# Kernel tuning notes

Hardware: AMD Instinct MI355X
Metric: run time of the kernel (lower is better)

The kernel has to match this reference:

```python
import jax, jax.numpy as jnp
import numpy as np

TEMPERATURE = 3.0
SINKHORN_ITERS = 20
NOISE_SCALE = 1.0
EPS = 1e-20


def setup_inputs() -> dict:
    key = jax.random.key(0)
    k1, k2, k3 = jax.random.split(key, 3)
    x = jax.random.normal(k1, (524288, 128), dtype=jnp.float32)
    logits = jax.random.normal(k2, (128, 128), dtype=jnp.float32)
    u = jax.random.uniform(k3, (128, 128), dtype=jnp.float32)
    return {"x": x, "logits": logits, "u": u}


def reference(x, logits, u):
    # Gumbel noise from uniform sample (matches sample_gumbel)
    gumbel = -jnp.log(-jnp.log(u + EPS) + EPS) * NOISE_SCALE
    log_alpha = (logits + gumbel) / TEMPERATURE
    log_alpha = jnp.clip(log_alpha, -10.0, 10.0)
    A = jnp.exp(log_alpha)
    # Sinkhorn: alternate row / column normalization (fixed 20 iters)
    for _ in range(SINKHORN_ITERS):
        A = A / jnp.sum(A, axis=1, keepdims=True)
        A = A / jnp.sum(A, axis=0, keepdims=True)
    P = jnp.nan_to_num(A, nan=0.0, posinf=1.0, neginf=0.0)
    # [batch, num_inputs] @ [num_inputs, num_leaves]
    return x @ P.T
```

## Files before the change

### kernel.cpp

```cpp
#include <hip/hip_runtime.h>
#include <hip/hip_bf16.h>

typedef _Float16 half8 __attribute__((ext_vector_type(8)));
typedef float floatx4 __attribute__((ext_vector_type(4)));

__global__ __launch_bounds__(256, 1) void sinkhorn128(
    const float* __restrict__ logits, const float* __restrict__ u,
    _Float16* __restrict__ Pout) {
    __shared__ float sA[128 * 129];
    __shared__ alignas(16) float sR[128];
    __shared__ alignas(16) float sC[128];
    const int t = threadIdx.x;
    const int i = t & 127;
    const bool isRow = (t < 128);

    float a[128];

    if (isRow) {
        #pragma unroll
        for (int j = 0; j < 128; ++j) {
            float lg = logits[i * 128 + j];
            float uu = u[i * 128 + j];
            float g  = -logf(-logf(uu + 1e-20f) + 1e-20f);
            float la = (lg + g) / 3.0f;
            la = fminf(10.0f, fmaxf(-10.0f, la));
            float v = expf(la);
            a[j] = v;
            sA[i * 129 + j] = v;
        }
        sC[i] = 1.0f;
    }
    __syncthreads();
    if (!isRow) {
        #pragma unroll
        for (int j = 0; j < 128; ++j) a[j] = sA[j * 129 + i];
    }

    float ri = 1.0f;
    for (int it = 0; it < 20; ++it) {
        if (isRow) {
            float s0 = 0.f, s1 = 0.f, s2 = 0.f, s3 = 0.f;
            #pragma unroll
            for (int j = 0; j < 128; j += 4) {
                float4 c4 = *reinterpret_cast<const float4*>(&sC[j]);
                s0 = fmaf(a[j + 0], c4.x, s0);
                s1 = fmaf(a[j + 1], c4.y, s1);
                s2 = fmaf(a[j + 2], c4.z, s2);
                s3 = fmaf(a[j + 3], c4.w, s3);
            }
            ri = 1.0f / ((s0 + s1) + (s2 + s3));
            sR[i] = ri;
        }
        __syncthreads();
        if (!isRow) {
            float s0 = 0.f, s1 = 0.f, s2 = 0.f, s3 = 0.f;
            #pragma unroll
            for (int j = 0; j < 128; j += 4) {
                float4 r4 = *reinterpret_cast<const float4*>(&sR[j]);
                s0 = fmaf(a[j + 0], r4.x, s0);
                s1 = fmaf(a[j + 1], r4.y, s1);
                s2 = fmaf(a[j + 2], r4.z, s2);
                s3 = fmaf(a[j + 3], r4.w, s3);
            }
            float ci = 1.0f / ((s0 + s1) + (s2 + s3));
            sC[i] = ci;
        }
        __syncthreads();
    }

    if (isRow) {
        #pragma unroll
        for (int j = 0; j < 128; j += 2) {
            union { _Float16 h[2]; unsigned int w; } pk;
            pk.h[0] = (_Float16)(ri * a[j + 0] * sC[j + 0]);
            pk.h[1] = (_Float16)(ri * a[j + 1] * sC[j + 1]);
            reinterpret_cast<unsigned int*>(Pout)[(i * 128 + j) >> 1] = pk.w;
        }
    }
}

__global__ __launch_bounds__(256, 2) void streamMatmul(
    const float* __restrict__ x, const _Float16* __restrict__ P,
    float* __restrict__ out) {
    const int lane = threadIdx.x & 63;
    const int wv   = threadIdx.x >> 6;
    const int gw   = blockIdx.x * 4 + wv;
    const int r    = lane & 15;
    const int q    = lane >> 4;

    half8 Bf[4][8];
    #pragma unroll
    for (int ks = 0; ks < 4; ++ks)
        #pragma unroll
        for (int nt = 0; nt < 8; ++nt)
            Bf[ks][nt] = *reinterpret_cast<const half8*>(
                P + (nt * 16 + r) * 128 + ks * 32 + q * 8);

    const long baseRow = (long)gw * 256;
    for (int t = 0; t < 16; ++t) {
        const long m0 = baseRow + t * 16;
        const float* xp = x + (m0 + r) * 128 + q * 8;

        floatx4 xa[4][2];
        #pragma unroll
        for (int ks = 0; ks < 4; ++ks) {
            xa[ks][0] = __builtin_nontemporal_load(
                reinterpret_cast<const floatx4*>(xp + ks * 32));
            xa[ks][1] = __builtin_nontemporal_load(
                reinterpret_cast<const floatx4*>(xp + ks * 32 + 4));
        }

        floatx4 acc[8];
        #pragma unroll
        for (int nt = 0; nt < 8; ++nt) acc[nt] = (floatx4){0.f, 0.f, 0.f, 0.f};

        #pragma unroll
        for (int ks = 0; ks < 4; ++ks) {
            half8 ahi, alo;
            #pragma unroll
            for (int jj = 0; jj < 8; ++jj) {
                float f = (jj < 4) ? xa[ks][0][jj] : xa[ks][1][jj - 4];
                _Float16 h = (_Float16)f;
                ahi[jj] = h;
                alo[jj] = (_Float16)(f - (float)h);
            }
            #pragma unroll
            for (int nt = 0; nt < 8; ++nt) {
                acc[nt] = __builtin_amdgcn_mfma_f32_16x16x32_f16(
                    ahi, Bf[ks][nt], acc[nt], 0, 0, 0);
                acc[nt] = __builtin_amdgcn_mfma_f32_16x16x32_f16(
                    alo, Bf[ks][nt], acc[nt], 0, 0, 0);
            }
        }

        float* op = out + (m0 + q * 4) * 128 + r;
        #pragma unroll
        for (int nt = 0; nt < 8; ++nt)
            #pragma unroll
            for (int rr = 0; rr < 4; ++rr)
                __builtin_nontemporal_store(acc[nt][rr], op + rr * 128 + nt * 16);
    }
}

extern "C" void kernel_launch(void* const* d_in, const int* in_sizes, int n_in,
                              void* d_out, int out_size, void* d_ws, size_t ws_size,
                              hipStream_t stream) {
    (void)in_sizes; (void)n_in; (void)out_size; (void)ws_size;
    const float* x      = (const float*)d_in[0];
    const float* logits = (const float*)d_in[1];
    const float* u      = (const float*)d_in[2];
    float* out          = (float*)d_out;
    _Float16* P         = (_Float16*)d_ws;

    sinkhorn128<<<1, 256, 0, stream>>>(logits, u, P);
    streamMatmul<<<512, 256, 0, stream>>>(x, P, out);
}
```

Before: 530.3 us.

## Parallelize Sinkhorn over 1024 threads and software-pipeline x loads in matmul

The Sinkhorn kernel now uses 1024 threads. The elementwise Gumbel/exp setup is spread over all threads, and each row or column sum is split across 4 lanes and combined with shuffle reductions. This shortens the serial single-block prologue, which had only 128 threads doing 128-long loops. The streaming matmul now prefetches the next tile of x into registers while running the MFMAs on the current one, and it drops the nontemporal loads. Launch bounds change to 1 block per SM, which may lower occupancy in exchange for more registers for the prefetch buffers.

```diff
diff --git a/kernel.cpp b/kernel.cpp
--- a/kernel.cpp
+++ b/kernel.cpp
@@ -4,36 +4,38 @@
 typedef _Float16 half8 __attribute__((ext_vector_type(8)));
 typedef float floatx4 __attribute__((ext_vector_type(4)));
 
-__global__ __launch_bounds__(256, 1) void sinkhorn128(
+__global__ __launch_bounds__(1024, 1) void sinkhorn128(
     const float* __restrict__ logits, const float* __restrict__ u,
     _Float16* __restrict__ Pout) {
     __shared__ float sA[128 * 129];
     __shared__ alignas(16) float sR[128];
     __shared__ alignas(16) float sC[128];
     const int t = threadIdx.x;
-    const int i = t & 127;
-    const bool isRow = (t < 128);
 
-    float a[128];
+    #pragma unroll
+    for (int k = 0; k < 16; ++k) {
+        int e = t + (k << 10);
+        float lg = logits[e];
+        float uu = u[e];
+        float g  = -logf(-logf(uu + 1e-20f) + 1e-20f);
+        float la = (lg + g) * (1.0f / 3.0f);
+        la = fminf(10.0f, fmaxf(-10.0f, la));
+        sA[(e >> 7) * 129 + (e & 127)] = expf(la);
+    }
+    if (t < 128) sC[t] = 1.0f;
+    __syncthreads();
 
+    const bool isRow = (t < 512);
+    const int i = (t & 511) >> 2;
+    const int q = t & 3;
+
+    float a[32];
     if (isRow) {
         #pragma unroll
-        for (int j = 0; j < 128; ++j) {
-            float lg = logits[i * 128 + j];
-            float uu = u[i * 128 + j];
-            float g  = -logf(-logf(uu + 1e-20f) + 1e-20f);
-            float la = (lg + g) / 3.0f;
-            la = fminf(10.0f, fmaxf(-10.0f, la));
-            float v = expf(la);
-            a[j] = v;
-            sA[i * 129 + j] = v;
-        }
-        sC[i] = 1.0f;
-    }
-    __syncthreads();
-    if (!isRow) {
+        for (int j = 0; j < 32; ++j) a[j] = sA[i * 129 + q * 32 + j];
+    } else {
         #pragma unroll
-        for (int j = 0; j < 128; ++j) a[j] = sA[j * 129 + i];
+        for (int j = 0; j < 32; ++j) a[j] = sA[(q * 32 + j) * 129 + i];
     }
 
     float ri = 1.0f;
@@ -41,45 +43,50 @@
         if (isRow) {
             float s0 = 0.f, s1 = 0.f, s2 = 0.f, s3 = 0.f;
             #pragma unroll
-            for (int j = 0; j < 128; j += 4) {
-                float4 c4 = *reinterpret_cast<const float4*>(&sC[j]);
+            for (int j = 0; j < 32; j += 4) {
+                float4 c4 = *reinterpret_cast<const float4*>(&sC[q * 32 + j]);
                 s0 = fmaf(a[j + 0], c4.x, s0);
                 s1 = fmaf(a[j + 1], c4.y, s1);
                 s2 = fmaf(a[j + 2], c4.z, s2);
                 s3 = fmaf(a[j + 3], c4.w, s3);
             }
-            ri = 1.0f / ((s0 + s1) + (s2 + s3));
-            sR[i] = ri;
+            float p = (s0 + s1) + (s2 + s3);
+            p += __shfl_xor(p, 1);
+            p += __shfl_xor(p, 2);
+            ri = 1.0f / p;
+            if (q == 0) sR[i] = ri;
         }
         __syncthreads();
         if (!isRow) {
             float s0 = 0.f, s1 = 0.f, s2 = 0.f, s3 = 0.f;
             #pragma unroll
-            for (int j = 0; j < 128; j += 4) {
-                float4 r4 = *reinterpret_cast<const float4*>(&sR[j]);
+            for (int j = 0; j < 32; j += 4) {
+                float4 r4 = *reinterpret_cast<const float4*>(&sR[q * 32 + j]);
                 s0 = fmaf(a[j + 0], r4.x, s0);
                 s1 = fmaf(a[j + 1], r4.y, s1);
                 s2 = fmaf(a[j + 2], r4.z, s2);
                 s3 = fmaf(a[j + 3], r4.w, s3);
             }
-            float ci = 1.0f / ((s0 + s1) + (s2 + s3));
-            sC[i] = ci;
+            float p = (s0 + s1) + (s2 + s3);
+            p += __shfl_xor(p, 1);
+            p += __shfl_xor(p, 2);
+            if (q == 0) sC[i] = 1.0f / p;
         }
         __syncthreads();
     }
 
     if (isRow) {
         #pragma unroll
-        for (int j = 0; j < 128; j += 2) {
+        for (int j = 0; j < 32; j += 2) {
             union { _Float16 h[2]; unsigned int w; } pk;
-            pk.h[0] = (_Float16)(ri * a[j + 0] * sC[j + 0]);
-            pk.h[1] = (_Float16)(ri * a[j + 1] * sC[j + 1]);
-            reinterpret_cast<unsigned int*>(Pout)[(i * 128 + j) >> 1] = pk.w;
+            pk.h[0] = (_Float16)(ri * a[j + 0] * sC[q * 32 + j + 0]);
+            pk.h[1] = (_Float16)(ri * a[j + 1] * sC[q * 32 + j + 1]);
+            reinterpret_cast<unsigned int*>(Pout)[(i * 128 + q * 32 + j) >> 1] = pk.w;
         }
     }
 }
 
-__global__ __launch_bounds__(256, 2) void streamMatmul(
+__global__ __launch_bounds__(256, 1) void streamMatmul(
     const float* __restrict__ x, const _Float16* __restrict__ P,
     float* __restrict__ out) {
     const int lane = threadIdx.x & 63;
@@ -97,17 +104,34 @@
                 P + (nt * 16 + r) * 128 + ks * 32 + q * 8);
 
     const long baseRow = (long)gw * 256;
+    const float* xp0 = x + (baseRow + r) * 128 + q * 8;
+
+    floatx4 xa[4][2];
+    #pragma unroll
+    for (int ks = 0; ks < 4; ++ks) {
+        xa[ks][0] = *reinterpret_cast<const floatx4*>(xp0 + ks * 32);
+        xa[ks][1] = *reinterpret_cast<const floatx4*>(xp0 + ks * 32 + 4);
+    }
+
     for (int t = 0; t < 16; ++t) {
-        const long m0 = baseRow + t * 16;
-        const float* xp = x + (m0 + r) * 128 + q * 8;
+        half8 ah[4], al[4];
+        #pragma unroll
+        for (int ks = 0; ks < 4; ++ks)
+            #pragma unroll
+            for (int jj = 0; jj < 8; ++jj) {
+                float f = (jj < 4) ? xa[ks][0][jj] : xa[ks][1][jj - 4];
+                _Float16 h = (_Float16)f;
+                ah[ks][jj] = h;
+                al[ks][jj] = (_Float16)(f - (float)h);
+            }
 
-        floatx4 xa[4][2];
-        #pragma unroll
-        for (int ks = 0; ks < 4; ++ks) {
-            xa[ks][0] = __builtin_nontemporal_load(
-                reinterpret_cast<const floatx4*>(xp + ks * 32));
-            xa[ks][1] = __builtin_nontemporal_load(
-                reinterpret_cast<const floatx4*>(xp + ks * 32 + 4));
+        if (t < 15) {
+            const float* xp = xp0 + (t + 1) * 16 * 128;
+            #pragma unroll
+            for (int ks = 0; ks < 4; ++ks) {
+                xa[ks][0] = *reinterpret_cast<const floatx4*>(xp + ks * 32);
+                xa[ks][1] = *reinterpret_cast<const floatx4*>(xp + ks * 32 + 4);
+            }
         }
 
         floatx4 acc[8];
@@ -115,24 +139,16 @@
         for (int nt = 0; nt < 8; ++nt) acc[nt] = (floatx4){0.f, 0.f, 0.f, 0.f};
 
         #pragma unroll
-        for (int ks = 0; ks < 4; ++ks) {
-            half8 ahi, alo;
-            #pragma unroll
-            for (int jj = 0; jj < 8; ++jj) {
-                float f = (jj < 4) ? xa[ks][0][jj] : xa[ks][1][jj - 4];
-                _Float16 h = (_Float16)f;
-                ahi[jj] = h;
-                alo[jj] = (_Float16)(f - (float)h);
-            }
+        for (int ks = 0; ks < 4; ++ks)
             #pragma unroll
             for (int nt = 0; nt < 8; ++nt) {
                 acc[nt] = __builtin_amdgcn_mfma_f32_16x16x32_f16(
-                    ahi, Bf[ks][nt], acc[nt], 0, 0, 0);
+                    ah[ks], Bf[ks][nt], acc[nt], 0, 0, 0);
                 acc[nt] = __builtin_amdgcn_mfma_f32_16x16x32_f16(
-                    alo, Bf[ks][nt], acc[nt], 0, 0, 0);
+                    al[ks], Bf[ks][nt], acc[nt], 0, 0, 0);
             }
-        }
 
+        const long m0 = baseRow + t * 16;
         float* op = out + (m0 + q * 4) * 128 + r;
         #pragma unroll
         for (int nt = 0; nt < 8; ++nt)
@@ -152,6 +168,6 @@
     float* out          = (float*)d_out;
     _Float16* P         = (_Float16*)d_ws;
 
-    sinkhorn128<<<1, 256, 0, stream>>>(logits, u, P);
+    sinkhorn128<<<1, 1024, 0, stream>>>(logits, u, P);
     streamMatmul<<<512, 256, 0, stream>>>(x, P, out);
 }
```

After: 494.0 us. -6.8%, faster.
